# Kernel optimization log

Hardware: AMD Instinct MI355X
Metric: run time of the kernel (lower is better)

## Reference

```python
import jax, jax.numpy as jnp
import numpy as np

G, B, T, D, U = 3, 32, 1024, 512, 512  # branches, batch, time, feat dim, units

def setup_inputs() -> dict:
    key = jax.random.key(0)
    ks = jax.random.split(key, 8)
    s = 0.02
    return {
        "query": jax.random.normal(ks[0], (G, B, D), jnp.float32),
        "values": jax.random.normal(ks[1], (G, B, T, D), jnp.float32),
        "W1": jax.random.normal(ks[2], (G, D, U), jnp.float32) * s,
        "b1": jnp.zeros((G, U), jnp.float32),
        "W2": jax.random.normal(ks[3], (G, D, U), jnp.float32) * s,
        "b2": jnp.zeros((G, U), jnp.float32),
        "V": jax.random.normal(ks[4], (G, U), jnp.float32) * s,
        "bV": jnp.zeros((G,), jnp.float32),
    }

def reference(query, values, W1, b1, W2, b2, V, bV):
    # query: [G,B,D], values: [G,B,T,D]; G=3 independent additive-attention branches.
    qp = jnp.einsum('gbd,gdu->gbu', query, W1) + b1[:, None, :]          # [G,B,U]
    vp = jnp.einsum('gbtd,gdu->gbtu', values, W2) + b2[:, None, None, :]  # [G,B,T,U]
    feat = jnp.tanh(qp[:, :, None, :] + vp)                               # [G,B,T,U]
    score = jnp.einsum('gbtu,gu->gbt', feat, V) + bV[:, None, None]       # [G,B,T]
    weights = jax.nn.softmax(score, axis=2)                               # softmax over time
    context = jnp.einsum('gbt,gbtd->gbd', weights, values)                # [G,B,D]
    return context, weights[..., None]  # matches tf.stack outputs: [3,B,D], [3,B,T,1]
```

## Files before the change

### kernel.cpp

```cpp
#include <hip/hip_runtime.h>
#include <cstdint>
#include <cstddef>

#define NG 3
#define NB 32
#define NT 1024
#define ND 512
#define NU 512

typedef __bf16 bf16x8 __attribute__((ext_vector_type(8)));
typedef float  f32x16 __attribute__((ext_vector_type(16)));

static __device__ __forceinline__ unsigned int f2bf(float f) {
    union { float f; unsigned int u; } v; v.f = f;
    return (v.u + 0x7FFFu + ((v.u >> 16) & 1u)) >> 16;
}

static __device__ __forceinline__ unsigned int cvt_pk_bf16(float lo, float hi) {
    unsigned int r;
    asm("v_cvt_pk_bf16_f32 %0, %1, %2" : "=v"(r) : "v"(lo), "v"(hi));
    return r;
}

static __device__ __forceinline__ bf16x8 ld_bf16x8(const char* base, int off) {
    return __builtin_bit_cast(bf16x8, *(const uint4*)(base + off));
}

#define AS1(p) ((const __attribute__((address_space(1))) void*)(p))
#define AS3(p) ((__attribute__((address_space(3))) void*)(p))

__global__ __launch_bounds__(256) void prep_qb_kernel(
    const float* __restrict__ query, const float* __restrict__ W1,
    const float* __restrict__ b1, const float* __restrict__ b2,
    float* __restrict__ qb)
{
    __shared__ float qs[NB][ND];
    const int g  = blockIdx.x >> 3;
    const int uc = blockIdx.x & 7;
    const int tid = threadIdx.x;

    const float4* qsrc = (const float4*)(query + (size_t)g * NB * ND);
    #pragma unroll
    for (int i = 0; i < 16; ++i)
        ((float4*)&qs[0][0])[tid + i * 256] = qsrc[tid + i * 256];
    __syncthreads();

    const int u  = uc * 64 + (tid & 63);
    const int b0 = tid >> 6;
    float acc[8] = {};
    const float* w1col = W1 + (size_t)g * ND * NU + u;
    for (int d = 0; d < ND; ++d) {
        float w = w1col[(size_t)d * NU];
        #pragma unroll
        for (int j = 0; j < 8; ++j)
            acc[j] = fmaf(qs[b0 + 4 * j][d], w, acc[j]);
    }
    const float bias = b1[g * NU + u] + b2[g * NU + u];
    #pragma unroll
    for (int j = 0; j < 8; ++j)
        qb[((size_t)g * NB + (b0 + 4 * j)) * NU + u] = acc[j] + bias;
}

__global__ __launch_bounds__(256) void prep_w2t_kernel(
    const float* __restrict__ W2, char* __restrict__ w2t)
{
    __shared__ float tile[64][65];
    const int g  = blockIdx.x >> 6;
    const int tb = blockIdx.x & 63;
    const int d0 = (tb >> 3) * 64;
    const int u0 = (tb & 7) * 64;
    const int tx = threadIdx.x & 63;
    const int ty = threadIdx.x >> 6;

    const float* src = W2 + (size_t)g * ND * NU;
    #pragma unroll
    for (int k = 0; k < 16; ++k) {
        int r = ty + 4 * k;
        tile[r][tx] = src[(size_t)(d0 + r) * NU + (u0 + tx)];
    }
    __syncthreads();
    char* dstg = w2t + (size_t)g * 16 * 32768;
    #pragma unroll
    for (int k = 0; k < 16; ++k) {
        int ul = ty + 4 * k;
        int u  = u0 + ul;
        int d  = d0 + tx;
        unsigned short h = (unsigned short)f2bf(tile[tx][ul]);
        int r  = u & 31;
        int kq = d >> 7;
        int kp = d & 127;
        size_t off = (size_t)(u >> 5) * 32768 + (size_t)kq * 8192
                   + (size_t)(r << 8)
                   + (size_t)(((kp << 1) ^ ((r & 7) << 4)));
        *(unsigned short*)(dstg + off) = h;
    }
}

__global__ __launch_bounds__(256, 2) void score_kernel(
    const float* __restrict__ values, const char* __restrict__ w2t,
    const float* __restrict__ qb, const float* __restrict__ Vvec,
    const float* __restrict__ bV, float* __restrict__ scores)
{
    __shared__ char  Bs[4][2][8192];
    __shared__ float qbs[NU];
    __shared__ float Vs[NU];

    const int blk = blockIdx.x;
    const int g   = blk >> 8;
    const int rem = blk & 255;
    const int b   = rem >> 3;
    const int t0  = (rem & 7) << 7;
    const int tid  = threadIdx.x;
    const int lane = tid & 63;
    const int wave = tid >> 6;

    const char* w2g = w2t + ((size_t)g << 19);

    auto stage = [&](int nuc, int nkq, char* dst) {
        const char* src = w2g + ((size_t)nuc << 15) + (nkq << 13) + (lane << 4);
        char* d = dst + (lane << 4);
        #pragma unroll
        for (int i = 0; i < 8; ++i)
            __builtin_amdgcn_global_load_lds(AS1(src + (i << 10)),
                                             AS3(d + (i << 10)), 16, 0, 0);
    };

    bf16x8 afrag[32];
    {
        const int arow_t = t0 + (wave << 5) + (lane & 31);
        const float* arow = values + (((size_t)g * NB + b) * NT + arow_t) * ND;
        const int acol = (lane >> 5) << 3;
        #pragma unroll
        for (int kk = 0; kk < 32; ++kk) {
            const float4* ap = (const float4*)(arow + (kk << 4) + acol);
            float4 v0 = ap[0], v1 = ap[1];
            union { bf16x8 v; unsigned int u[4]; } t;
            t.u[0] = cvt_pk_bf16(v0.x, v0.y);
            t.u[1] = cvt_pk_bf16(v0.z, v0.w);
            t.u[2] = cvt_pk_bf16(v1.x, v1.y);
            t.u[3] = cvt_pk_bf16(v1.z, v1.w);
            afrag[kk] = t.v;
        }
    }

    {
        const float* qsrc = qb + ((size_t)g * NB + b) * NU;
        const float* vsrc = Vvec + (size_t)g * NU;
        __builtin_amdgcn_global_load_lds(AS1(qsrc + tid),       AS3(&qbs[tid]),       4, 0, 0);
        __builtin_amdgcn_global_load_lds(AS1(qsrc + tid + 256), AS3(&qbs[tid + 256]), 4, 0, 0);
        __builtin_amdgcn_global_load_lds(AS1(vsrc + tid),       AS3(&Vs[tid]),        4, 0, 0);
        __builtin_amdgcn_global_load_lds(AS1(vsrc + tid + 256), AS3(&Vs[tid + 256]),  4, 0, 0);
    }

    char* myB0 = &Bs[wave][0][0];
    char* myB1 = &Bs[wave][1][0];
    stage(0, 0, myB0);

    asm volatile("s_waitcnt vmcnt(0) lgkmcnt(0)" ::: "memory");
    __builtin_amdgcn_s_barrier();

    const int brow  = lane & 31;
    const int h16   = (lane >> 5) << 4;
    const int bswz  = (brow & 7) << 4;
    const int bbase = brow << 8;

    float p[16] = {};

    #define PHASE(RB, AFBASE, NUC, NKQ, SB)                                      \
        stage((NUC), (NKQ), (SB));                                               \
        asm volatile("s_waitcnt vmcnt(8)" ::: "memory");                         \
        __builtin_amdgcn_sched_barrier(0);                                       \
        __builtin_amdgcn_s_setprio(1);                                           \
        _Pragma("unroll")                                                        \
        for (int j = 0; j < 8; ++j) {                                            \
            bf16x8 bb = ld_bf16x8((RB), bbase + ((((j) << 5) + h16) ^ bswz));    \
            acc = __builtin_amdgcn_mfma_f32_32x32x16_bf16(afrag[(AFBASE) + j],   \
                                                          bb, acc, 0, 0, 0);     \
        }                                                                        \
        __builtin_amdgcn_s_setprio(0);

    #pragma unroll 1
    for (int uc = 0; uc < 16; ++uc) {
        f32x16 acc = (f32x16)(0.0f);
        PHASE(myB0,  0, uc, 1, myB1)
        PHASE(myB1,  8, uc, 2, myB0)
        PHASE(myB0, 16, uc, 3, myB1)
        PHASE(myB1, 24, (uc + 1) & 15, 0, myB0)
        {
            const int u = (uc << 5) + brow;
            const float qv = qbs[u], vv = Vs[u];
            #pragma unroll
            for (int r = 0; r < 16; ++r) {
                float x  = acc[r] + qv;
                float e  = exp2f(2.8853900817779268f * x);
                float th = 1.0f - 2.0f * __builtin_amdgcn_rcpf(e + 1.0f);
                p[r] = fmaf(th, vv, p[r]);
            }
        }
    }
    #undef PHASE

    asm volatile("s_waitcnt vmcnt(0)" ::: "memory");

    #pragma unroll
    for (int r = 0; r < 16; ++r) {
        float v = p[r];
        v += __shfl_xor(v, 1);
        v += __shfl_xor(v, 2);
        v += __shfl_xor(v, 4);
        v += __shfl_xor(v, 8);
        v += __shfl_xor(v, 16);
        p[r] = v;
    }
    if ((lane & 31) == 0) {
        const float bv = bV[g];
        float* srow = scores + ((size_t)g * NB + b) * NT + t0 + (wave << 5);
        #pragma unroll
        for (int r = 0; r < 16; ++r) {
            int t_local = (r & 3) + 8 * (r >> 2) + 4 * (lane >> 5);
            srow[t_local] = p[r] + bv;
        }
    }
}

__global__ __launch_bounds__(256) void finish_kernel(
    const float* __restrict__ scores, const float* __restrict__ values,
    float* __restrict__ out_ctx, float* __restrict__ out_w)
{
    __shared__ float sl[NT];
    __shared__ float red[16];
    __shared__ float cred[4][128];
    const int blk   = blockIdx.x;
    const int gb    = blk >> 2;
    const int slice = blk & 3;
    const int tid = threadIdx.x;
    const int lane = tid & 63, wid = tid >> 6;

    const float* srow = scores + (size_t)gb * NT;
    float s[4];
    #pragma unroll
    for (int j = 0; j < 4; ++j) s[j] = srow[tid + 256 * j];

    float m = fmaxf(fmaxf(s[0], s[1]), fmaxf(s[2], s[3]));
    #pragma unroll
    for (int mask = 32; mask; mask >>= 1) m = fmaxf(m, __shfl_xor(m, mask));
    if (lane == 0) red[wid] = m;
    __syncthreads();
    const float gm = fmaxf(fmaxf(red[0], red[1]), fmaxf(red[2], red[3]));

    float e[4], ps = 0.f;
    #pragma unroll
    for (int j = 0; j < 4; ++j) { e[j] = __expf(s[j] - gm); ps += e[j]; }
    #pragma unroll
    for (int mask = 32; mask; mask >>= 1) ps += __shfl_xor(ps, mask);
    if (lane == 0) red[8 + wid] = ps;
    __syncthreads();
    const float inv = 1.f / (red[8] + red[9] + red[10] + red[11]);

    #pragma unroll
    for (int j = 0; j < 4; ++j) {
        float w = e[j] * inv;
        sl[tid + 256 * j] = w;
        if (slice == 0) out_w[(size_t)gb * NT + tid + 256 * j] = w;
    }
    __syncthreads();

    const int dp = tid & 63;
    const int tg = tid >> 6;
    const float* vbase = values + (size_t)gb * NT * ND + slice * 128 + dp * 2;
    float ax = 0.f, ay = 0.f;
    #pragma unroll 4
    for (int t = tg; t < NT; t += 4) {
        float2 v = *(const float2*)(vbase + (size_t)t * ND);
        float w = sl[t];
        ax = fmaf(w, v.x, ax);
        ay = fmaf(w, v.y, ay);
    }
    cred[tg][dp * 2]     = ax;
    cred[tg][dp * 2 + 1] = ay;
    __syncthreads();
    if (tid < 128) {
        float r = cred[0][tid] + cred[1][tid] + cred[2][tid] + cred[3][tid];
        out_ctx[(size_t)gb * ND + slice * 128 + tid] = r;
    }
}

extern "C" void kernel_launch(void* const* d_in, const int* in_sizes, int n_in,
                              void* d_out, int out_size, void* d_ws, size_t ws_size,
                              hipStream_t stream)
{
    (void)in_sizes; (void)n_in; (void)out_size; (void)ws_size;
    const float* query  = (const float*)d_in[0];
    const float* values = (const float*)d_in[1];
    const float* W1     = (const float*)d_in[2];
    const float* b1     = (const float*)d_in[3];
    const float* W2     = (const float*)d_in[4];
    const float* b2     = (const float*)d_in[5];
    const float* Vv     = (const float*)d_in[6];
    const float* bV     = (const float*)d_in[7];

    float* out_ctx = (float*)d_out;
    float* out_w   = out_ctx + (size_t)NG * NB * ND;

    float* qb     = (float*)d_ws;
    float* scores = qb + (size_t)NG * NB * NU;
    char*  w2t    = (char*)(scores + (size_t)NG * NB * NT);

    prep_qb_kernel <<<NG * 8,             256, 0, stream>>>(query, W1, b1, b2, qb);
    prep_w2t_kernel<<<NG * 64,            256, 0, stream>>>(W2, w2t);
    score_kernel   <<<NG * NB * (NT/128), 256, 0, stream>>>(values, w2t, qb, Vv, bV, scores);
    finish_kernel  <<<NG * NB * 4,        256, 0, stream>>>(scores, values, out_ctx, out_w);
}
```

Baseline: 169.5 us.

## Split score GEMM over U quarters with resident W2 tile and streamed A

```diff
diff --git a/kernel.cpp b/kernel.cpp
--- a/kernel.cpp
+++ b/kernel.cpp
@@ -7,6 +7,7 @@
 #define NT 1024
 #define ND 512
 #define NU 512
+#define PLANE (NG * NB * NT)
 
 typedef __bf16 bf16x8 __attribute__((ext_vector_type(8)));
 typedef float  f32x16 __attribute__((ext_vector_type(16)));
@@ -15,13 +16,15 @@
     union { float f; unsigned int u; } v; v.f = f;
     return (v.u + 0x7FFFu + ((v.u >> 16) & 1u)) >> 16;
 }
-
+static __device__ __forceinline__ float bf2f(unsigned short h) {
+    union { float f; unsigned int u; } v; v.u = ((unsigned int)h) << 16;
+    return v.f;
+}
 static __device__ __forceinline__ unsigned int cvt_pk_bf16(float lo, float hi) {
     unsigned int r;
     asm("v_cvt_pk_bf16_f32 %0, %1, %2" : "=v"(r) : "v"(lo), "v"(hi));
     return r;
 }
-
 static __device__ __forceinline__ bf16x8 ld_bf16x8(const char* base, int off) {
     return __builtin_bit_cast(bf16x8, *(const uint4*)(base + off));
 }
@@ -62,7 +65,7 @@
 }
 
 __global__ __launch_bounds__(256) void prep_w2t_kernel(
-    const float* __restrict__ W2, char* __restrict__ w2t)
+    const float* __restrict__ W2, unsigned short* __restrict__ w2t)
 {
     __shared__ float tile[64][65];
     const int g  = blockIdx.x >> 6;
@@ -79,152 +82,160 @@
         tile[r][tx] = src[(size_t)(d0 + r) * NU + (u0 + tx)];
     }
     __syncthreads();
-    char* dstg = w2t + (size_t)g * 16 * 32768;
     #pragma unroll
     for (int k = 0; k < 16; ++k) {
         int ul = ty + 4 * k;
         int u  = u0 + ul;
         int d  = d0 + tx;
         unsigned short h = (unsigned short)f2bf(tile[tx][ul]);
-        int r  = u & 31;
-        int kq = d >> 7;
-        int kp = d & 127;
-        size_t off = (size_t)(u >> 5) * 32768 + (size_t)kq * 8192
-                   + (size_t)(r << 8)
-                   + (size_t)(((kp << 1) ^ ((r & 7) << 4)));
-        *(unsigned short*)(dstg + off) = h;
-    }
-}
-
-__global__ __launch_bounds__(256, 2) void score_kernel(
-    const float* __restrict__ values, const char* __restrict__ w2t,
-    const float* __restrict__ qb, const float* __restrict__ Vvec,
-    const float* __restrict__ bV, float* __restrict__ scores)
-{
-    __shared__ char  Bs[4][2][8192];
-    __shared__ float qbs[NU];
-    __shared__ float Vs[NU];
-
-    const int blk = blockIdx.x;
-    const int g   = blk >> 8;
-    const int rem = blk & 255;
-    const int b   = rem >> 3;
-    const int t0  = (rem & 7) << 7;
+        int nq = u >> 7, u_l = u & 127, kg = d >> 3, e = d & 7;
+        size_t off_el = ((size_t)(g * 4 + nq) << 16)
+                      + (size_t)((kg << 10) + (u_l << 3) + e);
+        w2t[off_el] = h;
+    }
+}
+
+#define COMPUTE(AV_, KS_) do {                                                 \
+    const int _kb = ((KS_) << 14) + bconst;                                    \
+    _Pragma("unroll")                                                          \
+    for (int _kf = 0; _kf < 4; ++_kf) {                                        \
+        union { bf16x8 v; unsigned int u[4]; } _t;                             \
+        _t.u[0] = cvt_pk_bf16((AV_)[2*_kf].x,   (AV_)[2*_kf].y);               \
+        _t.u[1] = cvt_pk_bf16((AV_)[2*_kf].z,   (AV_)[2*_kf].w);               \
+        _t.u[2] = cvt_pk_bf16((AV_)[2*_kf+1].x, (AV_)[2*_kf+1].y);             \
+        _t.u[3] = cvt_pk_bf16((AV_)[2*_kf+1].z, (AV_)[2*_kf+1].w);             \
+        bf16x8 _b0 = ld_bf16x8(Bsc, _kb + (_kf << 12));                        \
+        bf16x8 _b1 = ld_bf16x8(Bsc, _kb + (_kf << 12) + 512);                  \
+        bf16x8 _b2 = ld_bf16x8(Bsc, _kb + (_kf << 12) + 1024);                 \
+        bf16x8 _b3 = ld_bf16x8(Bsc, _kb + (_kf << 12) + 1536);                 \
+        acc0 = __builtin_amdgcn_mfma_f32_32x32x16_bf16(_t.v, _b0, acc0, 0, 0, 0); \
+        acc1 = __builtin_amdgcn_mfma_f32_32x32x16_bf16(_t.v, _b1, acc1, 0, 0, 0); \
+        acc2 = __builtin_amdgcn_mfma_f32_32x32x16_bf16(_t.v, _b2, acc2, 0, 0, 0); \
+        acc3 = __builtin_amdgcn_mfma_f32_32x32x16_bf16(_t.v, _b3, acc3, 0, 0, 0); \
+    }                                                                          \
+} while (0)
+
+#define LOADA(AV_, MT_, KS_) do {                                             \
+    const float* _ap = abase + (MT_) * 131072 + ((KS_) << 6);                 \
+    _Pragma("unroll")                                                         \
+    for (int _kf = 0; _kf < 4; ++_kf) {                                       \
+        const float4* _p = (const float4*)(_ap + (_kf << 4));                 \
+        (AV_)[2*_kf] = _p[0]; (AV_)[2*_kf+1] = _p[1];                         \
+    }                                                                         \
+} while (0)
+
+#define EPI_UT(ACC_, UT_) do {                                                \
+    _Pragma("unroll")                                                         \
+    for (int _r = 0; _r < 16; ++_r) {                                         \
+        float _x = (ACC_)[_r] + qv[UT_];                                      \
+        float _e = exp2f(2.8853900817779268f * _x);                           \
+        float _t = 1.0f - 2.0f * __builtin_amdgcn_rcpf(_e + 1.0f);            \
+        p[_r] = fmaf(_t, vv[UT_], p[_r]);                                     \
+    }                                                                         \
+} while (0)
+
+__global__ __launch_bounds__(512) void score_kernel(
+    const float* __restrict__ values, const unsigned short* __restrict__ w2t,
+    const float* __restrict__ qbg, const float* __restrict__ Vvec,
+    unsigned short* __restrict__ parts)
+{
+    __shared__ char  Bs[131072];
+    __shared__ float qbs[128];
+    __shared__ float Vs[128];
+
+    const int blk  = blockIdx.x;
+    const int g    = blk >> 8;
+    const int rem  = blk & 255;
+    const int b    = rem >> 3;
+    const int th   = (rem >> 2) & 1;
+    const int nq   = rem & 3;
     const int tid  = threadIdx.x;
     const int lane = tid & 63;
     const int wave = tid >> 6;
-
-    const char* w2g = w2t + ((size_t)g << 19);
-
-    auto stage = [&](int nuc, int nkq, char* dst) {
-        const char* src = w2g + ((size_t)nuc << 15) + (nkq << 13) + (lane << 4);
-        char* d = dst + (lane << 4);
-        #pragma unroll
-        for (int i = 0; i < 8; ++i)
-            __builtin_amdgcn_global_load_lds(AS1(src + (i << 10)),
-                                             AS3(d + (i << 10)), 16, 0, 0);
-    };
-
-    bf16x8 afrag[32];
-    {
-        const int arow_t = t0 + (wave << 5) + (lane & 31);
-        const float* arow = values + (((size_t)g * NB + b) * NT + arow_t) * ND;
-        const int acol = (lane >> 5) << 3;
-        #pragma unroll
-        for (int kk = 0; kk < 32; ++kk) {
-            const float4* ap = (const float4*)(arow + (kk << 4) + acol);
-            float4 v0 = ap[0], v1 = ap[1];
-            union { bf16x8 v; unsigned int u[4]; } t;
-            t.u[0] = cvt_pk_bf16(v0.x, v0.y);
-            t.u[1] = cvt_pk_bf16(v0.z, v0.w);
-            t.u[2] = cvt_pk_bf16(v1.x, v1.y);
-            t.u[3] = cvt_pk_bf16(v1.z, v1.w);
-            afrag[kk] = t.v;
-        }
-    }
-
-    {
-        const float* qsrc = qb + ((size_t)g * NB + b) * NU;
-        const float* vsrc = Vvec + (size_t)g * NU;
-        __builtin_amdgcn_global_load_lds(AS1(qsrc + tid),       AS3(&qbs[tid]),       4, 0, 0);
-        __builtin_amdgcn_global_load_lds(AS1(qsrc + tid + 256), AS3(&qbs[tid + 256]), 4, 0, 0);
-        __builtin_amdgcn_global_load_lds(AS1(vsrc + tid),       AS3(&Vs[tid]),        4, 0, 0);
-        __builtin_amdgcn_global_load_lds(AS1(vsrc + tid + 256), AS3(&Vs[tid + 256]),  4, 0, 0);
-    }
-
-    char* myB0 = &Bs[wave][0][0];
-    char* myB1 = &Bs[wave][1][0];
-    stage(0, 0, myB0);
+    const int rl   = lane & 31;
+    const int hi   = lane >> 5;
+
+    const char* bimg = (const char*)w2t + ((size_t)(g * 4 + nq) << 17);
+    #pragma unroll
+    for (int ps = 0; ps < 16; ++ps)
+        __builtin_amdgcn_global_load_lds(AS1(bimg + (ps << 13) + (tid << 4)),
+                                         AS3(Bs + (ps << 13) + (tid << 4)), 16, 0, 0);
+    if (wave < 2) {
+        const float* qsrc = qbg + (((size_t)(g * NB + b)) << 9) + (nq << 7) + (wave << 6) + lane;
+        __builtin_amdgcn_global_load_lds(AS1(qsrc), AS3(&qbs[(wave << 6) + lane]), 4, 0, 0);
+    } else if (wave < 4) {
+        const float* vsrc = Vvec + (g << 9) + (nq << 7) + ((wave - 2) << 6) + lane;
+        __builtin_amdgcn_global_load_lds(AS1(vsrc), AS3(&Vs[((wave - 2) << 6) + lane]), 4, 0, 0);
+    }
+
+    const float* abase = values
+        + (((size_t)(g * NB + b) * NT) + th * 512 + (wave << 5) + rl) * ND + (hi << 3);
+
+    float4 av0[8], av1[8];
+    LOADA(av0, 0, 0);
 
     asm volatile("s_waitcnt vmcnt(0) lgkmcnt(0)" ::: "memory");
     __builtin_amdgcn_s_barrier();
 
-    const int brow  = lane & 31;
-    const int h16   = (lane >> 5) << 4;
-    const int bswz  = (brow & 7) << 4;
-    const int bbase = brow << 8;
-
-    float p[16] = {};
-
-    #define PHASE(RB, AFBASE, NUC, NKQ, SB)                                      \
-        stage((NUC), (NKQ), (SB));                                               \
-        asm volatile("s_waitcnt vmcnt(8)" ::: "memory");                         \
-        __builtin_amdgcn_sched_barrier(0);                                       \
-        __builtin_amdgcn_s_setprio(1);                                           \
-        _Pragma("unroll")                                                        \
-        for (int j = 0; j < 8; ++j) {                                            \
-            bf16x8 bb = ld_bf16x8((RB), bbase + ((((j) << 5) + h16) ^ bswz));    \
-            acc = __builtin_amdgcn_mfma_f32_32x32x16_bf16(afrag[(AFBASE) + j],   \
-                                                          bb, acc, 0, 0, 0);     \
-        }                                                                        \
-        __builtin_amdgcn_s_setprio(0);
+    float qv[4], vv[4];
+    #pragma unroll
+    for (int ut = 0; ut < 4; ++ut) {
+        qv[ut] = qbs[(ut << 5) + rl];
+        vv[ut] = Vs[(ut << 5) + rl];
+    }
+
+    const char* Bsc = Bs;
+    const int bconst = (hi << 11) + (rl << 4);
+
+    f32x16 acc0 = (f32x16)(0.0f), acc1 = (f32x16)(0.0f);
+    f32x16 acc2 = (f32x16)(0.0f), acc3 = (f32x16)(0.0f);
+
+    unsigned short* prow = parts + (size_t)nq * PLANE + ((size_t)(g * NB + b)) * NT;
 
     #pragma unroll 1
-    for (int uc = 0; uc < 16; ++uc) {
-        f32x16 acc = (f32x16)(0.0f);
-        PHASE(myB0,  0, uc, 1, myB1)
-        PHASE(myB1,  8, uc, 2, myB0)
-        PHASE(myB0, 16, uc, 3, myB1)
-        PHASE(myB1, 24, (uc + 1) & 15, 0, myB0)
-        {
-            const int u = (uc << 5) + brow;
-            const float qv = qbs[u], vv = Vs[u];
+    for (int s2 = 0; s2 < 8; ++s2) {
+        const int mt  = s2 >> 2;
+        const int ksE = (2 * s2) & 7;
+        const int ksO = ksE + 1;
+
+        LOADA(av1, mt, ksO);
+        COMPUTE(av0, ksE);
+
+        if (s2 < 7) {
+            const int mtN = (s2 + 1) >> 2;
+            const int ksN = (2 * s2 + 2) & 7;
+            LOADA(av0, mtN, ksN);
+        }
+        COMPUTE(av1, ksO);
+
+        if (s2 == 3 || s2 == 7) {
+            float p[16] = {};
+            EPI_UT(acc0, 0); EPI_UT(acc1, 1); EPI_UT(acc2, 2); EPI_UT(acc3, 3);
             #pragma unroll
             for (int r = 0; r < 16; ++r) {
-                float x  = acc[r] + qv;
-                float e  = exp2f(2.8853900817779268f * x);
-                float th = 1.0f - 2.0f * __builtin_amdgcn_rcpf(e + 1.0f);
-                p[r] = fmaf(th, vv, p[r]);
+                float v = p[r];
+                v += __shfl_xor(v, 1);
+                v += __shfl_xor(v, 2);
+                v += __shfl_xor(v, 4);
+                v += __shfl_xor(v, 8);
+                v += __shfl_xor(v, 16);
+                p[r] = v;
             }
+            if (rl == 0) {
+                const int trow = th * 512 + mt * 256 + (wave << 5) + 4 * hi;
+                #pragma unroll
+                for (int r = 0; r < 16; ++r)
+                    prow[trow + (r & 3) + 8 * (r >> 2)] = (unsigned short)f2bf(p[r]);
+            }
+            acc0 = (f32x16)(0.0f); acc1 = (f32x16)(0.0f);
+            acc2 = (f32x16)(0.0f); acc3 = (f32x16)(0.0f);
         }
     }
-    #undef PHASE
-
-    asm volatile("s_waitcnt vmcnt(0)" ::: "memory");
-
-    #pragma unroll
-    for (int r = 0; r < 16; ++r) {
-        float v = p[r];
-        v += __shfl_xor(v, 1);
-        v += __shfl_xor(v, 2);
-        v += __shfl_xor(v, 4);
-        v += __shfl_xor(v, 8);
-        v += __shfl_xor(v, 16);
-        p[r] = v;
-    }
-    if ((lane & 31) == 0) {
-        const float bv = bV[g];
-        float* srow = scores + ((size_t)g * NB + b) * NT + t0 + (wave << 5);
-        #pragma unroll
-        for (int r = 0; r < 16; ++r) {
-            int t_local = (r & 3) + 8 * (r >> 2) + 4 * (lane >> 5);
-            srow[t_local] = p[r] + bv;
-        }
-    }
 }
 
 __global__ __launch_bounds__(256) void finish_kernel(
-    const float* __restrict__ scores, const float* __restrict__ values,
+    const unsigned short* __restrict__ parts, const float* __restrict__ bV,
+    const float* __restrict__ values,
     float* __restrict__ out_ctx, float* __restrict__ out_w)
 {
     __shared__ float sl[NT];
@@ -235,11 +246,15 @@
     const int slice = blk & 3;
     const int tid = threadIdx.x;
     const int lane = tid & 63, wid = tid >> 6;
-
-    const float* srow = scores + (size_t)gb * NT;
+    const float bv = bV[gb >> 5];
+
     float s[4];
     #pragma unroll
-    for (int j = 0; j < 4; ++j) s[j] = srow[tid + 256 * j];
+    for (int j = 0; j < 4; ++j) {
+        size_t idx = (size_t)gb * NT + tid + 256 * j;
+        s[j] = bf2f(parts[idx]) + bf2f(parts[idx + PLANE])
+             + bf2f(parts[idx + 2 * PLANE]) + bf2f(parts[idx + 3 * PLANE]) + bv;
+    }
 
     float m = fmaxf(fmaxf(s[0], s[1]), fmaxf(s[2], s[3]));
     #pragma unroll
@@ -302,12 +317,12 @@
     float* out_ctx = (float*)d_out;
     float* out_w   = out_ctx + (size_t)NG * NB * ND;
 
-    float* qb     = (float*)d_ws;
-    float* scores = qb + (size_t)NG * NB * NU;
-    char*  w2t    = (char*)(scores + (size_t)NG * NB * NT);
-
-    prep_qb_kernel <<<NG * 8,             256, 0, stream>>>(query, W1, b1, b2, qb);
-    prep_w2t_kernel<<<NG * 64,            256, 0, stream>>>(W2, w2t);
-    score_kernel   <<<NG * NB * (NT/128), 256, 0, stream>>>(values, w2t, qb, Vv, bV, scores);
-    finish_kernel  <<<NG * NB * 4,        256, 0, stream>>>(scores, values, out_ctx, out_w);
-}
+    float* qb = (float*)d_ws;
+    unsigned short* parts = (unsigned short*)(qb + (size_t)NG * NB * NU);
+    unsigned short* w2t   = parts + (size_t)4 * PLANE;
+
+    prep_qb_kernel <<<NG * 8,      256, 0, stream>>>(query, W1, b1, b2, qb);
+    prep_w2t_kernel<<<NG * 64,     256, 0, stream>>>(W2, w2t);
+    score_kernel   <<<NG * 256,    512, 0, stream>>>(values, w2t, qb, Vv, parts);
+    finish_kernel  <<<NG * NB * 4, 256, 0, stream>>>(parts, bV, values, out_ctx, out_w);
+}
```

Result: slower. 190.7 us (+12.5%).

## Restructure score kernel to 16x16 MFMA with shared block-wide triple-buffered W2 staging

Applied to the files above, without the earlier changes.

```diff
diff --git a/kernel.cpp b/kernel.cpp
--- a/kernel.cpp
+++ b/kernel.cpp
@@ -9,19 +9,17 @@
 #define NU 512
 
 typedef __bf16 bf16x8 __attribute__((ext_vector_type(8)));
-typedef float  f32x16 __attribute__((ext_vector_type(16)));
+typedef float  f32x4  __attribute__((ext_vector_type(4)));
 
 static __device__ __forceinline__ unsigned int f2bf(float f) {
     union { float f; unsigned int u; } v; v.f = f;
     return (v.u + 0x7FFFu + ((v.u >> 16) & 1u)) >> 16;
 }
-
 static __device__ __forceinline__ unsigned int cvt_pk_bf16(float lo, float hi) {
     unsigned int r;
     asm("v_cvt_pk_bf16_f32 %0, %1, %2" : "=v"(r) : "v"(lo), "v"(hi));
     return r;
 }
-
 static __device__ __forceinline__ bf16x8 ld_bf16x8(const char* base, int off) {
     return __builtin_bit_cast(bf16x8, *(const uint4*)(base + off));
 }
@@ -79,61 +77,68 @@
         tile[r][tx] = src[(size_t)(d0 + r) * NU + (u0 + tx)];
     }
     __syncthreads();
-    char* dstg = w2t + (size_t)g * 16 * 32768;
     #pragma unroll
     for (int k = 0; k < 16; ++k) {
         int ul = ty + 4 * k;
         int u  = u0 + ul;
         int d  = d0 + tx;
         unsigned short h = (unsigned short)f2bf(tile[tx][ul]);
-        int r  = u & 31;
-        int kq = d >> 7;
-        int kp = d & 127;
-        size_t off = (size_t)(u >> 5) * 32768 + (size_t)kq * 8192
-                   + (size_t)(r << 8)
-                   + (size_t)(((kp << 1) ^ ((r & 7) << 4)));
-        *(unsigned short*)(dstg + off) = h;
-    }
-}
-
-__global__ __launch_bounds__(256, 2) void score_kernel(
+        int uc   = u >> 5, u32 = u & 31;
+        int nf   = u32 >> 4, u16 = u32 & 15;
+        int kq   = d >> 7, kk32 = (d >> 5) & 3, kgrp = (d >> 3) & 3, e = d & 7;
+        size_t off = ((size_t)((g * 16 + uc) * 4 + kq) << 13)
+                   + (size_t)((kk32 << 11) + (nf << 10) + (u16 << 6) + (kgrp << 4) + (e << 1));
+        *(unsigned short*)(w2t + off) = h;
+    }
+}
+
+__global__ __launch_bounds__(256, 4) void score_kernel(
     const float* __restrict__ values, const char* __restrict__ w2t,
-    const float* __restrict__ qb, const float* __restrict__ Vvec,
-    const float* __restrict__ bV, float* __restrict__ scores)
-{
-    __shared__ char  Bs[4][2][8192];
+    const float* __restrict__ qbg, const float* __restrict__ Vvec,
+    float* __restrict__ scores)
+{
+    __shared__ char  Bs[3][8192];
     __shared__ float qbs[NU];
     __shared__ float Vs[NU];
 
-    const int blk = blockIdx.x;
-    const int g   = blk >> 8;
-    const int rem = blk & 255;
-    const int b   = rem >> 3;
-    const int t0  = (rem & 7) << 7;
+    const int blk  = blockIdx.x;
+    const int g    = blk >> 9;
+    const int rem  = blk & 511;
+    const int b    = rem >> 4;
+    const int t0   = (rem & 15) << 6;
     const int tid  = threadIdx.x;
     const int lane = tid & 63;
     const int wave = tid >> 6;
+    const int row16 = lane & 15;
+    const int kg    = lane >> 4;
 
     const char* w2g = w2t + ((size_t)g << 19);
 
-    auto stage = [&](int nuc, int nkq, char* dst) {
-        const char* src = w2g + ((size_t)nuc << 15) + (nkq << 13) + (lane << 4);
-        char* d = dst + (lane << 4);
+    auto stage = [&](int ph, char* buf) {
+        const char* src = w2g + ((size_t)ph << 13) + (tid << 4);
+        __builtin_amdgcn_global_load_lds(AS1(src),        AS3(buf + (tid << 4)),        16, 0, 0);
+        __builtin_amdgcn_global_load_lds(AS1(src + 4096), AS3(buf + (tid << 4) + 4096), 16, 0, 0);
+    };
+
+    {
+        const float* qsrc = qbg + ((size_t)(g * NB + b)) * NU;
+        const float* vsrc = Vvec + (size_t)g * NU;
+        __builtin_amdgcn_global_load_lds(AS1(qsrc + tid),       AS3(&qbs[tid]),       4, 0, 0);
+        __builtin_amdgcn_global_load_lds(AS1(qsrc + tid + 256), AS3(&qbs[tid + 256]), 4, 0, 0);
+        __builtin_amdgcn_global_load_lds(AS1(vsrc + tid),       AS3(&Vs[tid]),        4, 0, 0);
+        __builtin_amdgcn_global_load_lds(AS1(vsrc + tid + 256), AS3(&Vs[tid + 256]),  4, 0, 0);
+    }
+    stage(0, Bs[0]);
+    stage(1, Bs[1]);
+
+    bf16x8 afrag[16];
+    {
+        const float* aptr = values
+            + ((size_t)((g * NB + b) * NT + t0 + (wave << 4) + row16)) * ND + (kg << 3);
         #pragma unroll
-        for (int i = 0; i < 8; ++i)
-            __builtin_amdgcn_global_load_lds(AS1(src + (i << 10)),
-                                             AS3(d + (i << 10)), 16, 0, 0);
-    };
-
-    bf16x8 afrag[32];
-    {
-        const int arow_t = t0 + (wave << 5) + (lane & 31);
-        const float* arow = values + (((size_t)g * NB + b) * NT + arow_t) * ND;
-        const int acol = (lane >> 5) << 3;
-        #pragma unroll
-        for (int kk = 0; kk < 32; ++kk) {
-            const float4* ap = (const float4*)(arow + (kk << 4) + acol);
-            float4 v0 = ap[0], v1 = ap[1];
+        for (int kk = 0; kk < 16; ++kk) {
+            const float4* p4 = (const float4*)(aptr + (kk << 5));
+            float4 v0 = p4[0], v1 = p4[1];
             union { bf16x8 v; unsigned int u[4]; } t;
             t.u[0] = cvt_pk_bf16(v0.x, v0.y);
             t.u[1] = cvt_pk_bf16(v0.z, v0.w);
@@ -143,88 +148,84 @@
         }
     }
 
-    {
-        const float* qsrc = qb + ((size_t)g * NB + b) * NU;
-        const float* vsrc = Vvec + (size_t)g * NU;
-        __builtin_amdgcn_global_load_lds(AS1(qsrc + tid),       AS3(&qbs[tid]),       4, 0, 0);
-        __builtin_amdgcn_global_load_lds(AS1(qsrc + tid + 256), AS3(&qbs[tid + 256]), 4, 0, 0);
-        __builtin_amdgcn_global_load_lds(AS1(vsrc + tid),       AS3(&Vs[tid]),        4, 0, 0);
-        __builtin_amdgcn_global_load_lds(AS1(vsrc + tid + 256), AS3(&Vs[tid + 256]),  4, 0, 0);
-    }
-
-    char* myB0 = &Bs[wave][0][0];
-    char* myB1 = &Bs[wave][1][0];
-    stage(0, 0, myB0);
-
     asm volatile("s_waitcnt vmcnt(0) lgkmcnt(0)" ::: "memory");
     __builtin_amdgcn_s_barrier();
 
-    const int brow  = lane & 31;
-    const int h16   = (lane >> 5) << 4;
-    const int bswz  = (brow & 7) << 4;
-    const int bbase = brow << 8;
-
-    float p[16] = {};
-
-    #define PHASE(RB, AFBASE, NUC, NKQ, SB)                                      \
-        stage((NUC), (NKQ), (SB));                                               \
-        asm volatile("s_waitcnt vmcnt(8)" ::: "memory");                         \
-        __builtin_amdgcn_sched_barrier(0);                                       \
-        __builtin_amdgcn_s_setprio(1);                                           \
-        _Pragma("unroll")                                                        \
-        for (int j = 0; j < 8; ++j) {                                            \
-            bf16x8 bb = ld_bf16x8((RB), bbase + ((((j) << 5) + h16) ^ bswz));    \
-            acc = __builtin_amdgcn_mfma_f32_32x32x16_bf16(afrag[(AFBASE) + j],   \
-                                                          bb, acc, 0, 0, 0);     \
-        }                                                                        \
-        __builtin_amdgcn_s_setprio(0);
+    const int bconst = (row16 << 6) + (kg << 4);
+    f32x4 acc0 = (f32x4)(0.0f);
+    f32x4 acc1 = (f32x4)(0.0f);
+    float p[4] = {};
+
+    char* ba = (char*)Bs[0];
+    char* bb = (char*)Bs[1];
+    char* bc = (char*)Bs[2];
+
+    #define PHASE(KQ_) do {                                                       \
+        const int _ph = (uc << 2) + (KQ_);                                        \
+        if (_ph < 62) stage(_ph + 2, bc);                                         \
+        __builtin_amdgcn_s_setprio(1);                                            \
+        _Pragma("unroll")                                                         \
+        for (int _i = 0; _i < 4; ++_i) {                                          \
+            bf16x8 _b0 = ld_bf16x8(ba, (_i << 11) + bconst);                      \
+            bf16x8 _b1 = ld_bf16x8(ba, (_i << 11) + 1024 + bconst);               \
+            acc0 = __builtin_amdgcn_mfma_f32_16x16x32_bf16(                       \
+                       afrag[((KQ_) << 2) + _i], _b0, acc0, 0, 0, 0);             \
+            acc1 = __builtin_amdgcn_mfma_f32_16x16x32_bf16(                       \
+                       afrag[((KQ_) << 2) + _i], _b1, acc1, 0, 0, 0);             \
+        }                                                                         \
+        __builtin_amdgcn_s_setprio(0);                                            \
+        if ((KQ_) == 3) {                     \
+            const int _ub = uc << 5;                                              \
+            float _qv0 = qbs[_ub + row16],      _vv0 = Vs[_ub + row16];           \
+            float _qv1 = qbs[_ub + 16 + row16], _vv1 = Vs[_ub + 16 + row16];      \
+            _Pragma("unroll")                                                     \
+            for (int _r = 0; _r < 4; ++_r) {                                      \
+                float _x0 = acc0[_r] + _qv0;                                      \
+                float _e0 = exp2f(2.8853900817779268f * _x0);                     \
+                float _t0 = 1.0f - 2.0f * __builtin_amdgcn_rcpf(_e0 + 1.0f);      \
+                p[_r] = fmaf(_t0, _vv0, p[_r]);                                   \
+                float _x1 = acc1[_r] + _qv1;                                      \
+                float _e1 = exp2f(2.8853900817779268f * _x1);                     \
+                float _t1 = 1.0f - 2.0f * __builtin_amdgcn_rcpf(_e1 + 1.0f);      \
+                p[_r] = fmaf(_t1, _vv1, p[_r]);                                   \
+            }                                                                     \
+            acc0 = (f32x4)(0.0f); acc1 = (f32x4)(0.0f);                           \
+        }                                                                         \
+        if (_ph < 62)       { asm volatile("s_waitcnt vmcnt(2)" ::: "memory"); }  \
+        else if (_ph == 62) { asm volatile("s_waitcnt vmcnt(0)" ::: "memory"); }  \
+        if (_ph < 63) __builtin_amdgcn_s_barrier();                               \
+        { char* _t = ba; ba = bb; bb = bc; bc = _t; }                             \
+    } while (0)
 
     #pragma unroll 1
     for (int uc = 0; uc < 16; ++uc) {
-        f32x16 acc = (f32x16)(0.0f);
-        PHASE(myB0,  0, uc, 1, myB1)
-        PHASE(myB1,  8, uc, 2, myB0)
-        PHASE(myB0, 16, uc, 3, myB1)
-        PHASE(myB1, 24, (uc + 1) & 15, 0, myB0)
-        {
-            const int u = (uc << 5) + brow;
-            const float qv = qbs[u], vv = Vs[u];
-            #pragma unroll
-            for (int r = 0; r < 16; ++r) {
-                float x  = acc[r] + qv;
-                float e  = exp2f(2.8853900817779268f * x);
-                float th = 1.0f - 2.0f * __builtin_amdgcn_rcpf(e + 1.0f);
-                p[r] = fmaf(th, vv, p[r]);
-            }
-        }
+        PHASE(0);
+        PHASE(1);
+        PHASE(2);
+        PHASE(3);
     }
     #undef PHASE
 
-    asm volatile("s_waitcnt vmcnt(0)" ::: "memory");
-
-    #pragma unroll
-    for (int r = 0; r < 16; ++r) {
+    #pragma unroll
+    for (int r = 0; r < 4; ++r) {
         float v = p[r];
         v += __shfl_xor(v, 1);
         v += __shfl_xor(v, 2);
         v += __shfl_xor(v, 4);
         v += __shfl_xor(v, 8);
-        v += __shfl_xor(v, 16);
         p[r] = v;
     }
-    if ((lane & 31) == 0) {
-        const float bv = bV[g];
-        float* srow = scores + ((size_t)g * NB + b) * NT + t0 + (wave << 5);
+    if (row16 == 0) {
+        float* srow = scores + ((size_t)(g * NB + b)) * NT + t0 + (wave << 4);
         #pragma unroll
-        for (int r = 0; r < 16; ++r) {
-            int t_local = (r & 3) + 8 * (r >> 2) + 4 * (lane >> 5);
-            srow[t_local] = p[r] + bv;
-        }
+        for (int r = 0; r < 4; ++r)
+            srow[(kg << 2) + r] = p[r];
     }
 }
 
 __global__ __launch_bounds__(256) void finish_kernel(
-    const float* __restrict__ scores, const float* __restrict__ values,
+    const float* __restrict__ scores, const float* __restrict__ bV,
+    const float* __restrict__ values,
     float* __restrict__ out_ctx, float* __restrict__ out_w)
 {
     __shared__ float sl[NT];
@@ -235,11 +236,12 @@
     const int slice = blk & 3;
     const int tid = threadIdx.x;
     const int lane = tid & 63, wid = tid >> 6;
-
-    const float* srow = scores + (size_t)gb * NT;
+    const float bv = bV[gb >> 5];
+
     float s[4];
     #pragma unroll
-    for (int j = 0; j < 4; ++j) s[j] = srow[tid + 256 * j];
+    for (int j = 0; j < 4; ++j)
+        s[j] = scores[(size_t)gb * NT + tid + 256 * j] + bv;
 
     float m = fmaxf(fmaxf(s[0], s[1]), fmaxf(s[2], s[3]));
     #pragma unroll
@@ -306,8 +308,8 @@
     float* scores = qb + (size_t)NG * NB * NU;
     char*  w2t    = (char*)(scores + (size_t)NG * NB * NT);
 
-    prep_qb_kernel <<<NG * 8,             256, 0, stream>>>(query, W1, b1, b2, qb);
-    prep_w2t_kernel<<<NG * 64,            256, 0, stream>>>(W2, w2t);
-    score_kernel   <<<NG * NB * (NT/128), 256, 0, stream>>>(values, w2t, qb, Vv, bV, scores);
-    finish_kernel  <<<NG * NB * 4,        256, 0, stream>>>(scores, values, out_ctx, out_w);
-}
+    prep_qb_kernel <<<NG * 8,            256, 0, stream>>>(query, W1, b1, b2, qb);
+    prep_w2t_kernel<<<NG * 64,           256, 0, stream>>>(W2, w2t);
+    score_kernel   <<<NG * NB * (NT/64), 256, 0, stream>>>(values, w2t, qb, Vv, scores);
+    finish_kernel  <<<NG * NB * 4,       256, 0, stream>>>(scores, bV, values, out_ctx, out_w);
+}
```

Result: faster. 159.4 us (-5.9%).
